# Optimization experiments

Hardware: AMD Instinct MI355X
Metric: run time of the kernel (lower is better)

Reference implementation:

```python
import jax, jax.numpy as jnp
import numpy as np

N, B, SD, ED = 2048, 64, 512, 512


def setup_inputs() -> dict:
    key = jax.random.key(0)
    k1, k2, k3 = jax.random.split(key, 3)
    state_tm1 = jax.random.normal(k1, (B, SD), dtype=jnp.float32)
    embeddings = jax.random.normal(k2, (N, B, ED), dtype=jnp.float32)
    W = jax.random.normal(k3, (SD + ED, 1), dtype=jnp.float32) * 0.02
    b = jnp.zeros((1,), dtype=jnp.float32)
    return {"state_tm1": state_tm1, "embeddings": embeddings, "W": W, "b": b}


def reference(state_tm1, embeddings, W, b):
    # fc(concat(state, emb)) == state @ W_s + emb @ W_e + b  (split the weight)
    sd = state_tm1.shape[1]
    W_s, W_e = W[:sd], W[sd:]                      # [SD,1], [ED,1]
    state_score = state_tm1 @ W_s + b              # [B,1]
    logits = jnp.einsum('nbe,eo->nbo', embeddings, W_e) + state_score  # [N,B,1]
    alphas = jax.nn.softmax(logits, axis=0)        # softmax over items (dim 0)
    # weighted sum over items: [B, ED]
    return jnp.einsum('nbo,nbe->be', alphas, embeddings)
```

## Files before the change

### kernel.cpp

```cpp
#include <hip/hip_runtime.h>
#include <math.h>

#define BCOL 64
#define ED 512
#define NROWS 2048

__global__ void attn_partial_kernel(const float* __restrict__ emb,
                                    const float* __restrict__ W,
                                    float* __restrict__ accbuf,
                                    float* __restrict__ mbuf,
                                    float* __restrict__ lbuf,
                                    int G, int rowsPerWave)
{
    const int tid  = threadIdx.x;
    const int lane = tid & 63;
    const int wv   = tid >> 6;
    const int blk  = blockIdx.x;
    const int col  = blk % BCOL;
    const int chunk = blk / BCOL;
    const int g = chunk * 4 + wv;
    const int n0 = g * rowsPerWave;

    const float4* We4 = (const float4*)(W + 512);
    const float4 w0 = We4[lane];
    const float4 w1 = We4[lane + 64];

    float m = -INFINITY, l = 0.0f;
    float4 acc0 = {0.f, 0.f, 0.f, 0.f};
    float4 acc1 = {0.f, 0.f, 0.f, 0.f};

    const float4* row = (const float4*)(emb + ((size_t)n0 * BCOL + col) * ED);
    float4 a0 = row[lane];
    float4 a1 = row[lane + 64];

    for (int i = 0; i < rowsPerWave; ++i) {
        float4 b0, b1;
        if (i + 1 < rowsPerWave) {
            const float4* nrow =
                (const float4*)(emb + ((size_t)(n0 + i + 1) * BCOL + col) * ED);
            b0 = nrow[lane];
            b1 = nrow[lane + 64];
        }
        float p = a0.x * w0.x + a0.y * w0.y + a0.z * w0.z + a0.w * w0.w
                + a1.x * w1.x + a1.y * w1.y + a1.z * w1.z + a1.w * w1.w;
        #pragma unroll
        for (int off = 32; off > 0; off >>= 1)
            p += __shfl_xor(p, off, 64);
        const float s = p;

        const float mn   = fmaxf(m, s);
        const float corr = __expf(m - mn);
        const float pe   = __expf(s - mn);
        l = l * corr + pe;
        acc0.x = acc0.x * corr + pe * a0.x;
        acc0.y = acc0.y * corr + pe * a0.y;
        acc0.z = acc0.z * corr + pe * a0.z;
        acc0.w = acc0.w * corr + pe * a0.w;
        acc1.x = acc1.x * corr + pe * a1.x;
        acc1.y = acc1.y * corr + pe * a1.y;
        acc1.z = acc1.z * corr + pe * a1.z;
        acc1.w = acc1.w * corr + pe * a1.w;
        m = mn;

        a0 = b0;
        a1 = b1;
    }

    float4* out4 = (float4*)(accbuf + ((size_t)col * G + g) * ED);
    out4[lane]      = acc0;
    out4[lane + 64] = acc1;
    if (lane == 0) {
        mbuf[col * G + g] = m;
        lbuf[col * G + g] = l;
    }
}

__global__ void attn_reduce_kernel(const float* __restrict__ accbuf,
                                   const float* __restrict__ mbuf,
                                   const float* __restrict__ lbuf,
                                   float* __restrict__ out,
                                   int G)
{
    const int b    = blockIdx.x >> 1;
    const int half = blockIdx.x & 1;
    const int tid  = threadIdx.x;

    __shared__ float sc[64];
    if (tid < 64) {
        float mg = (tid < G) ? mbuf[b * G + tid] : -INFINITY;
        float lg = (tid < G) ? lbuf[b * G + tid] : 0.0f;
        float M = mg;
        #pragma unroll
        for (int off = 32; off > 0; off >>= 1)
            M = fmaxf(M, __shfl_xor(M, off, 64));
        float el = lg * __expf(mg - M);
        float L = el;
        #pragma unroll
        for (int off = 32; off > 0; off >>= 1)
            L += __shfl_xor(L, off, 64);
        sc[tid] = __expf(mg - M) / L;
    }
    __syncthreads();

    const int e = half * 256 + tid;
    float s = 0.0f;
    for (int gg = 0; gg < G; ++gg)
        s += sc[gg] * accbuf[((size_t)b * G + gg) * ED + e];
    out[(size_t)b * ED + e] = s;
}

extern "C" void kernel_launch(void* const* d_in, const int* in_sizes, int n_in,
                              void* d_out, int out_size, void* d_ws, size_t ws_size,
                              hipStream_t stream) {
    const float* emb = (const float*)d_in[1];
    const float* W   = (const float*)d_in[2];
    float* out = (float*)d_out;

    int G = 64;
    while (G > 4) {
        size_t need = (size_t)BCOL * G * ED * sizeof(float)
                    + 2 * (size_t)BCOL * G * sizeof(float);
        if (need <= ws_size) break;
        G >>= 1;
    }
    const int rowsPerWave = NROWS / G;

    float* accbuf = (float*)d_ws;
    float* mbuf = accbuf + (size_t)BCOL * G * ED;
    float* lbuf = mbuf + BCOL * G;

    attn_partial_kernel<<<dim3(BCOL * (G / 4)), dim3(256), 0, stream>>>(
        emb, W, accbuf, mbuf, lbuf, G, rowsPerWave);
    attn_reduce_kernel<<<dim3(BCOL * 2), dim3(256), 0, stream>>>(
        accbuf, mbuf, lbuf, out, G);
}
```

Measured before the change: 368.2 us.

## Process four rows per online-softmax step with deeper prefetch and fixed G

The partial kernel now loads and scores four embedding rows per iteration and prefetches the next four, so one max/correction update covers four rows and more loads are in flight per wave. G is fixed at 64 at compile time instead of being chosen from workspace size, and launch bounds are set. The reduce kernel splits its sum over four accumulators. This raises memory-level parallelism for a bandwidth-bound stream, at the cost of more registers per thread and no fallback if the workspace is smaller than the fixed G requires.

Measured after the change: 420.6 us. +14.2%, slower.

```diff
diff --git a/kernel.cpp b/kernel.cpp
--- a/kernel.cpp
+++ b/kernel.cpp
@@ -4,66 +4,91 @@
 #define BCOL 64
 #define ED 512
 #define NROWS 2048
+#define G 64
+#define RPW (NROWS / G)
+#define RSTEP 4
 
-__global__ void attn_partial_kernel(const float* __restrict__ emb,
-                                    const float* __restrict__ W,
-                                    float* __restrict__ accbuf,
-                                    float* __restrict__ mbuf,
-                                    float* __restrict__ lbuf,
-                                    int G, int rowsPerWave)
+__global__ __launch_bounds__(256, 4)
+void attn_partial_kernel(const float* __restrict__ emb,
+                         const float* __restrict__ W,
+                         float* __restrict__ accbuf,
+                         float* __restrict__ mbuf,
+                         float* __restrict__ lbuf)
 {
     const int tid  = threadIdx.x;
     const int lane = tid & 63;
     const int wv   = tid >> 6;
-    const int blk  = blockIdx.x;
-    const int col  = blk % BCOL;
-    const int chunk = blk / BCOL;
+    const int col  = blockIdx.x & (BCOL - 1);
+    const int chunk = blockIdx.x >> 6;
     const int g = chunk * 4 + wv;
-    const int n0 = g * rowsPerWave;
+    const int n0 = g * RPW;
 
     const float4* We4 = (const float4*)(W + 512);
     const float4 w0 = We4[lane];
     const float4 w1 = We4[lane + 64];
 
     float m = -INFINITY, l = 0.0f;
-    float4 acc0 = {0.f, 0.f, 0.f, 0.f};
-    float4 acc1 = {0.f, 0.f, 0.f, 0.f};
+    float4 acc0 = {0.f,0.f,0.f,0.f}, acc1 = {0.f,0.f,0.f,0.f};
 
-    const float4* row = (const float4*)(emb + ((size_t)n0 * BCOL + col) * ED);
-    float4 a0 = row[lane];
-    float4 a1 = row[lane + 64];
+    const size_t rowStride = (size_t)BCOL * ED;
+    const float* base = emb + ((size_t)n0 * BCOL + col) * ED;
 
-    for (int i = 0; i < rowsPerWave; ++i) {
-        float4 b0, b1;
-        if (i + 1 < rowsPerWave) {
-            const float4* nrow =
-                (const float4*)(emb + ((size_t)(n0 + i + 1) * BCOL + col) * ED);
-            b0 = nrow[lane];
-            b1 = nrow[lane + 64];
+    float4 a[RSTEP][2], b[RSTEP][2];
+    #pragma unroll
+    for (int r = 0; r < RSTEP; ++r) {
+        const float4* rp = (const float4*)(base + (size_t)r * rowStride);
+        a[r][0] = rp[lane];
+        a[r][1] = rp[lane + 64];
+    }
+
+    for (int i = 0; i < RPW; i += RSTEP) {
+        const bool more = (i + RSTEP) < RPW;
+        if (more) {
+            #pragma unroll
+            for (int r = 0; r < RSTEP; ++r) {
+                const float4* rp = (const float4*)(base + (size_t)(i + RSTEP + r) * rowStride);
+                b[r][0] = rp[lane];
+                b[r][1] = rp[lane + 64];
+            }
         }
-        float p = a0.x * w0.x + a0.y * w0.y + a0.z * w0.z + a0.w * w0.w
-                + a1.x * w1.x + a1.y * w1.y + a1.z * w1.z + a1.w * w1.w;
+
+        float p[RSTEP];
         #pragma unroll
-        for (int off = 32; off > 0; off >>= 1)
-            p += __shfl_xor(p, off, 64);
-        const float s = p;
+        for (int r = 0; r < RSTEP; ++r) {
+            p[r] = a[r][0].x*w0.x + a[r][0].y*w0.y + a[r][0].z*w0.z + a[r][0].w*w0.w
+                 + a[r][1].x*w1.x + a[r][1].y*w1.y + a[r][1].z*w1.z + a[r][1].w*w1.w;
+        }
+        #pragma unroll
+        for (int off = 32; off > 0; off >>= 1) {
+            #pragma unroll
+            for (int r = 0; r < RSTEP; ++r)
+                p[r] += __shfl_xor(p[r], off, 64);
+        }
 
-        const float mn   = fmaxf(m, s);
+        const float mn = fmaxf(m, fmaxf(fmaxf(p[0], p[1]), fmaxf(p[2], p[3])));
         const float corr = __expf(m - mn);
-        const float pe   = __expf(s - mn);
-        l = l * corr + pe;
-        acc0.x = acc0.x * corr + pe * a0.x;
-        acc0.y = acc0.y * corr + pe * a0.y;
-        acc0.z = acc0.z * corr + pe * a0.z;
-        acc0.w = acc0.w * corr + pe * a0.w;
-        acc1.x = acc1.x * corr + pe * a1.x;
-        acc1.y = acc1.y * corr + pe * a1.y;
-        acc1.z = acc1.z * corr + pe * a1.z;
-        acc1.w = acc1.w * corr + pe * a1.w;
+        float pe[RSTEP];
+        #pragma unroll
+        for (int r = 0; r < RSTEP; ++r) pe[r] = __expf(p[r] - mn);
+        l = l * corr + ((pe[0] + pe[1]) + (pe[2] + pe[3]));
+
+        #pragma unroll
+        for (int h = 0; h < 2; ++h) {
+            float4& acc = h ? acc1 : acc0;
+            acc.x = acc.x*corr + pe[0]*a[0][h].x + pe[1]*a[1][h].x + pe[2]*a[2][h].x + pe[3]*a[3][h].x;
+            acc.y = acc.y*corr + pe[0]*a[0][h].y + pe[1]*a[1][h].y + pe[2]*a[2][h].y + pe[3]*a[3][h].y;
+            acc.z = acc.z*corr + pe[0]*a[0][h].z + pe[1]*a[1][h].z + pe[2]*a[2][h].z + pe[3]*a[3][h].z;
+            acc.w = acc.w*corr + pe[0]*a[0][h].w + pe[1]*a[1][h].w + pe[2]*a[2][h].w + pe[3]*a[3][h].w;
+        }
         m = mn;
 
-        a0 = b0;
-        a1 = b1;
+        if (more) {
+            #pragma unroll
+            for (int r = 0; r < RSTEP; ++r) {
+                a[r][0] = b[r][0];
+                a[r][1] = b[r][1];
+            }
+        }
     }
 
     float4* out4 = (float4*)(accbuf + ((size_t)col * G + g) * ED);
@@ -78,17 +103,16 @@
 __global__ void attn_reduce_kernel(const float* __restrict__ accbuf,
                                    const float* __restrict__ mbuf,
                                    const float* __restrict__ lbuf,
-                                   float* __restrict__ out,
-                                   int G)
+                                   float* __restrict__ out)
 {
     const int b    = blockIdx.x >> 1;
     const int half = blockIdx.x & 1;
     const int tid  = threadIdx.x;
 
-    __shared__ float sc[64];
+    __shared__ float sc[G];
     if (tid < 64) {
-        float mg = (tid < G) ? mbuf[b * G + tid] : -INFINITY;
-        float lg = (tid < G) ? lbuf[b * G + tid] : 0.0f;
+        float mg = mbuf[b * G + tid];
+        float lg = lbuf[b * G + tid];
         float M = mg;
         #pragma unroll
         for (int off = 32; off > 0; off >>= 1)
@@ -103,10 +127,16 @@
     __syncthreads();
 
     const int e = half * 256 + tid;
-    float s = 0.0f;
-    for (int gg = 0; gg < G; ++gg)
-        s += sc[gg] * accbuf[((size_t)b * G + gg) * ED + e];
-    out[(size_t)b * ED + e] = s;
+    const float* basep = accbuf + (size_t)b * G * ED + e;
+    float s0 = 0.f, s1 = 0.f, s2 = 0.f, s3 = 0.f;
+    #pragma unroll 1
+    for (int gg = 0; gg < G; gg += 4) {
+        s0 += sc[gg + 0] * basep[(size_t)(gg + 0) * ED];
+        s1 += sc[gg + 1] * basep[(size_t)(gg + 1) * ED];
+        s2 += sc[gg + 2] * basep[(size_t)(gg + 2) * ED];
+        s3 += sc[gg + 3] * basep[(size_t)(gg + 3) * ED];
+    }
+    out[(size_t)b * ED + e] = (s0 + s1) + (s2 + s3);
 }
 
 extern "C" void kernel_launch(void* const* d_in, const int* in_sizes, int n_in,
@@ -116,21 +146,12 @@
     const float* W   = (const float*)d_in[2];
     float* out = (float*)d_out;
 
-    int G = 64;
-    while (G > 4) {
-        size_t need = (size_t)BCOL * G * ED * sizeof(float)
-                    + 2 * (size_t)BCOL * G * sizeof(float);
-        if (need <= ws_size) break;
-        G >>= 1;
-    }
-    const int rowsPerWave = NROWS / G;
-
     float* accbuf = (float*)d_ws;
     float* mbuf = accbuf + (size_t)BCOL * G * ED;
     float* lbuf = mbuf + BCOL * G;
 
     attn_partial_kernel<<<dim3(BCOL * (G / 4)), dim3(256), 0, stream>>>(
-        emb, W, accbuf, mbuf, lbuf, G, rowsPerWave);
+        emb, W, accbuf, mbuf, lbuf);
     attn_reduce_kernel<<<dim3(BCOL * 2), dim3(256), 0, stream>>>(
-        accbuf, mbuf, lbuf, out, G);
+        accbuf, mbuf, lbuf, out);
 }
```
